# Optimization experiments

Hardware: AMD Instinct MI355X
Metric: run time of the kernel (lower is better)

Reference implementation:

```python
import jax, jax.numpy as jnp
import numpy as np

B, NQ, NK, D = 4, 512, 1024, 64
SCALE = 1.0


def _xavier(key, fan_in, fan_out):
    lim = np.sqrt(6.0 / (fan_in + fan_out))
    return jax.random.uniform(key, (fan_in, fan_out), jnp.float32, -lim, lim)


def setup_inputs() -> dict:
    key = jax.random.key(0)
    ks = jax.random.split(key, 7)
    return {
        "x1": jax.random.normal(ks[0], (B, NK, D), jnp.float32),   # context x -> keys
        "x2": jax.random.normal(ks[1], (B, NQ, D), jnp.float32),   # target x  -> queries
        "r":  jax.random.normal(ks[2], (B, NK, D), jnp.float32),   # values
        # key-path MLP (linear_layers_list): Linear(64,64) -> relu -> Linear(64,64)
        "Wk1": _xavier(ks[3], D, D), "bk1": jnp.zeros((D,), jnp.float32),
        "Wk2": _xavier(ks[4], D, D), "bk2": jnp.zeros((D,), jnp.float32),
        # query-path MLP (linear_layers_list2)
        "Wq1": _xavier(ks[5], D, D), "bq1": jnp.zeros((D,), jnp.float32),
        "Wq2": _xavier(ks[6], D, D), "bq2": jnp.zeros((D,), jnp.float32),
    }


def _mlp(x, W1, b1, W2, b2):
    # relu on all layers except the last (matches the torch loop)
    h = jax.nn.relu(jnp.einsum('bsd,de->bse', x, W1) + b1)
    return jnp.einsum('bsd,de->bse', h, W2) + b2


def reference(x1, x2, r, Wk1, bk1, Wk2, bk2, Wq1, bq1, Wq2, bq2):
    k = _mlp(x1, Wk1, bk1, Wk2, bk2)          # [B, NK, D]
    q = _mlp(x2, Wq1, bq1, Wq2, bq2)          # [B, NQ, D]
    # laplace attention: -sum_d |(k - q)/scale|, broadcast [B, NQ, NK, D]
    unnorm = -jnp.sum(jnp.abs((k[:, None, :, :] - q[:, :, None, :]) / SCALE), axis=-1)  # [B, NQ, NK]
    weights = jax.nn.softmax(unnorm, axis=2)  # normalise=True -> softmax over keys
    return jnp.einsum('bik,bkj->bij', weights, r)  # [B, NQ, D]
```

## Files before the change

kernel.cpp:

```cpp
#include <hip/hip_runtime.h>
#include <math.h>

#define BB 4
#define NQ 512
#define NK 1024
#define DH 64
#define TQ 8
#define TK 128
#define NCHUNK (NK / TK)
#define KPAD 65

__global__ __launch_bounds__(64) void mlp_kernel(
    const float* __restrict__ x1, const float* __restrict__ x2,
    const float* __restrict__ Wk1, const float* __restrict__ bk1,
    const float* __restrict__ Wk2, const float* __restrict__ bk2,
    const float* __restrict__ Wq1, const float* __restrict__ bq1,
    const float* __restrict__ Wq2, const float* __restrict__ bq2,
    float* __restrict__ kout, float* __restrict__ qout)
{
    const int row  = blockIdx.x;
    const int lane = threadIdx.x;
    const float *x, *W1, *b1, *W2, *b2;
    float* out;
    if (row < BB * NK) {
        x = x1 + row * DH;
        W1 = Wk1; b1 = bk1; W2 = Wk2; b2 = bk2;
        out = kout + row * DH;
    } else {
        const int rq = row - BB * NK;
        x = x2 + rq * DH;
        W1 = Wq1; b1 = bq1; W2 = Wq2; b2 = bq2;
        out = qout + rq * DH;
    }
    __shared__ float xs[DH];
    __shared__ float hs[DH];
    xs[lane] = x[lane];
    __syncthreads();
    float acc = b1[lane];
    #pragma unroll
    for (int d = 0; d < DH; ++d) acc = fmaf(xs[d], W1[d * DH + lane], acc);
    hs[lane] = fmaxf(acc, 0.0f);
    __syncthreads();
    float acc2 = b2[lane];
    #pragma unroll
    for (int d = 0; d < DH; ++d) acc2 = fmaf(hs[d], W2[d * DH + lane], acc2);
    out[lane] = acc2;
}

__global__ __launch_bounds__(512) void attn_kernel(
    const float* __restrict__ kmat, const float* __restrict__ qmat,
    const float* __restrict__ rmat, float* __restrict__ outp)
{
    __shared__ float k_s[TK * KPAD];
    __shared__ float p_s[TQ * TK];
    __shared__ float alpha_s[TQ];
    __shared__ float linv_s[TQ];

    const int t    = threadIdx.x;
    const int lane = t & 63;
    const int wav  = __builtin_amdgcn_readfirstlane(t >> 6);

    const int b  = blockIdx.x / (NQ / TQ);
    const int qt = blockIdx.x % (NQ / TQ);
    const int i0 = qt * TQ;

    const float* qrow = qmat + (b * NQ + i0 + wav) * DH;
    float qreg[DH];
    #pragma unroll
    for (int d = 0; d < DH; ++d) qreg[d] = qrow[d];

    const float* kbase = kmat + (size_t)b * NK * DH;
    const float* rbase = rmat + (size_t)b * NK * DH;

    float M_run = -INFINITY;
    float l_run = 0.0f;
    float O[TQ];
    #pragma unroll
    for (int i = 0; i < TQ; ++i) O[i] = 0.0f;

    for (int c = 0; c < NCHUNK; ++c) {
        const float4* ksrc = (const float4*)(kbase + c * TK * DH);
        #pragma unroll
        for (int rep = 0; rep < (TK * DH) / (512 * 4); ++rep) {
            int idx4 = rep * 512 + t;
            float4 v = ksrc[idx4];
            int e  = idx4 * 4;
            int jj = e >> 6;
            int dd = e & 63;
            float* dst = &k_s[jj * KPAD + dd];
            dst[0] = v.x; dst[1] = v.y; dst[2] = v.z; dst[3] = v.w;
        }
        __syncthreads();

        float s0 = 0.0f, s1 = 0.0f;
        #pragma unroll
        for (int d = 0; d < DH; ++d) {
            float q = qreg[d];
            s0 += fabsf(k_s[lane * KPAD + d] - q);
            s1 += fabsf(k_s[(lane + 64) * KPAD + d] - q);
        }
        float sm0 = -s0, sm1 = -s1;

        float cmax = fmaxf(sm0, sm1);
        #pragma unroll
        for (int off = 32; off > 0; off >>= 1)
            cmax = fmaxf(cmax, __shfl_xor(cmax, off, 64));
        float M_new = fmaxf(M_run, cmax);
        float p0 = __expf(sm0 - M_new);
        float p1 = __expf(sm1 - M_new);
        float csum = p0 + p1;
        #pragma unroll
        for (int off = 32; off > 0; off >>= 1)
            csum += __shfl_xor(csum, off, 64);
        float alpha = __expf(M_run - M_new);
        l_run = l_run * alpha + csum;
        M_run = M_new;
        p_s[wav * TK + lane]      = p0;
        p_s[wav * TK + lane + 64] = p1;
        if (lane == 0) alpha_s[wav] = alpha;
        __syncthreads();

        #pragma unroll
        for (int i = 0; i < TQ; ++i) O[i] *= alpha_s[i];
        const float* rc = rbase + c * TK * DH;
        #pragma unroll
        for (int jj = 0; jj < TK / 8; ++jj) {
            int j = wav * (TK / 8) + jj;
            float rv = rc[j * DH + lane];
            #pragma unroll
            for (int i = 0; i < TQ; ++i)
                O[i] = fmaf(p_s[i * TK + j], rv, O[i]);
        }
        __syncthreads();
    }

    if (lane == 0) linv_s[wav] = 1.0f / l_run;
    float* part = k_s;
    #pragma unroll
    for (int i = 0; i < TQ; ++i)
        part[(wav * TQ + i) * 64 + lane] = O[i];
    __syncthreads();

    float sum = 0.0f;
    #pragma unroll
    for (int g = 0; g < 8; ++g)
        sum += part[(g * TQ + wav) * 64 + lane];
    sum *= linv_s[wav];
    outp[((size_t)b * NQ + i0 + wav) * DH + lane] = sum;
}

extern "C" void kernel_launch(void* const* d_in, const int* in_sizes, int n_in,
                              void* d_out, int out_size, void* d_ws, size_t ws_size,
                              hipStream_t stream) {
    const float* x1  = (const float*)d_in[0];
    const float* x2  = (const float*)d_in[1];
    const float* r   = (const float*)d_in[2];
    const float* Wk1 = (const float*)d_in[3];
    const float* bk1 = (const float*)d_in[4];
    const float* Wk2 = (const float*)d_in[5];
    const float* bk2 = (const float*)d_in[6];
    const float* Wq1 = (const float*)d_in[7];
    const float* bq1 = (const float*)d_in[8];
    const float* Wq2 = (const float*)d_in[9];
    const float* bq2 = (const float*)d_in[10];
    float* out  = (float*)d_out;

    float* kbuf = (float*)d_ws;
    float* qbuf = kbuf + (size_t)BB * NK * DH;

    mlp_kernel<<<BB * (NK + NQ), 64, 0, stream>>>(
        x1, x2, Wk1, bk1, Wk2, bk2, Wq1, bq1, Wq2, bq2, kbuf, qbuf);

    attn_kernel<<<BB * (NQ / TQ), 512, 0, stream>>>(kbuf, qbuf, r, out);
}
```

Measured before the change: 111.1 us.

## Transpose K/Q layout and compute all scores per wave without online softmax

The MLP kernel now writes K and Q transposed (d-major), so the attention kernel can read K directly from global memory as coalesced float2 and reuse each K value across all 8 queries. The chunked online softmax with LDS staging of K is replaced by a single pass: each wave computes distances for 128 keys across 8 queries, a block-wide min reduction, and full exp into a 32KB p_s buffer, followed by a P·R pass. This removes per-chunk barriers and alpha rescaling and cuts the distance work from one query per wave to eight. In exchange the MLP stores become strided (uncoalesced), and the larger LDS footprint may lower occupancy.

```diff
diff --git a/kernel.cpp b/kernel.cpp
--- a/kernel.cpp
+++ b/kernel.cpp
@@ -6,9 +6,8 @@
 #define NK 1024
 #define DH 64
 #define TQ 8
-#define TK 128
-#define NCHUNK (NK / TK)
-#define KPAD 65
+#define NWAVE 8
+#define KPW (NK / NWAVE)
 
 __global__ __launch_bounds__(64) void mlp_kernel(
     const float* __restrict__ x1, const float* __restrict__ x2,
@@ -16,22 +15,26 @@
     const float* __restrict__ Wk2, const float* __restrict__ bk2,
     const float* __restrict__ Wq1, const float* __restrict__ bq1,
     const float* __restrict__ Wq2, const float* __restrict__ bq2,
-    float* __restrict__ kout, float* __restrict__ qout)
+    float* __restrict__ kT, float* __restrict__ qT)
 {
     const int row  = blockIdx.x;
     const int lane = threadIdx.x;
     const float *x, *W1, *b1, *W2, *b2;
     float* out;
     if (row < BB * NK) {
+        const int b = row / NK, j = row % NK;
         x = x1 + row * DH;
         W1 = Wk1; b1 = bk1; W2 = Wk2; b2 = bk2;
-        out = kout + row * DH;
+        out = kT + (size_t)b * DH * NK + j;
     } else {
         const int rq = row - BB * NK;
+        const int b = rq / NQ, i = rq % NQ;
         x = x2 + rq * DH;
         W1 = Wq1; b1 = bq1; W2 = Wq2; b2 = bq2;
-        out = qout + rq * DH;
+        out = qT + (size_t)b * DH * NQ + i;
     }
+    const int ostride = (row < BB * NK) ? NK : NQ;
+
     __shared__ float xs[DH];
     __shared__ float hs[DH];
     xs[lane] = x[lane];
@@ -44,98 +47,103 @@
     float acc2 = b2[lane];
     #pragma unroll
     for (int d = 0; d < DH; ++d) acc2 = fmaf(hs[d], W2[d * DH + lane], acc2);
-    out[lane] = acc2;
+    out[lane * ostride] = acc2;
 }
 
 __global__ __launch_bounds__(512) void attn_kernel(
-    const float* __restrict__ kmat, const float* __restrict__ qmat,
+    const float* __restrict__ kT, const float* __restrict__ qT,
     const float* __restrict__ rmat, float* __restrict__ outp)
 {
-    __shared__ float k_s[TK * KPAD];
-    __shared__ float p_s[TQ * TK];
-    __shared__ float alpha_s[TQ];
-    __shared__ float linv_s[TQ];
+    __shared__ float p_s[TQ * NK];
+    __shared__ float wmin_s[NWAVE * TQ];
+    __shared__ float wsum_s[NWAVE * TQ];
 
     const int t    = threadIdx.x;
     const int lane = t & 63;
     const int wav  = __builtin_amdgcn_readfirstlane(t >> 6);
 
     const int b  = blockIdx.x / (NQ / TQ);
-    const int qt = blockIdx.x % (NQ / TQ);
-    const int i0 = qt * TQ;
+    const int i0 = (blockIdx.x % (NQ / TQ)) * TQ;
 
-    const float* qrow = qmat + (b * NQ + i0 + wav) * DH;
-    float qreg[DH];
+    const float* kTb = kT + (size_t)b * DH * NK;
+    const float* qTb = qT + (size_t)b * DH * NQ;
+
+    const int j0 = wav * KPW + 2 * lane;
+
+    float s0[TQ], s1[TQ];
     #pragma unroll
-    for (int d = 0; d < DH; ++d) qreg[d] = qrow[d];
+    for (int i = 0; i < TQ; ++i) { s0[i] = 0.0f; s1[i] = 0.0f; }
 
-    const float* kbase = kmat + (size_t)b * NK * DH;
-    const float* rbase = rmat + (size_t)b * NK * DH;
+    #pragma unroll 8
+    for (int d = 0; d < DH; ++d) {
+        const float2 kv = *(const float2*)&kTb[d * NK + j0];
+        const float* qrow = qTb + d * NQ + i0;
+        #pragma unroll
+        for (int i = 0; i < TQ; ++i) {
+            const float q = qrow[i];
+            s0[i] += fabsf(kv.x - q);
+            s1[i] += fabsf(kv.y - q);
+        }
+    }
 
-    float M_run = -INFINITY;
-    float l_run = 0.0f;
+    #pragma unroll
+    for (int i = 0; i < TQ; ++i) {
+        float m = fminf(s0[i], s1[i]);
+        #pragma unroll
+        for (int off = 32; off > 0; off >>= 1)
+            m = fminf(m, __shfl_xor(m, off, 64));
+        if (lane == 0) wmin_s[wav * TQ + i] = m;
+    }
+    __syncthreads();
+
+    float M[TQ];
+    #pragma unroll
+    for (int i = 0; i < TQ; ++i) {
+        float m = wmin_s[i];
+        #pragma unroll
+        for (int g = 1; g < NWAVE; ++g) m = fminf(m, wmin_s[g * TQ + i]);
+        M[i] = m;
+    }
+
+    #pragma unroll
+    for (int i = 0; i < TQ; ++i) {
+        const float p0 = __expf(M[i] - s0[i]);
+        const float p1 = __expf(M[i] - s1[i]);
+        *(float2*)&p_s[i * NK + j0] = make_float2(p0, p1);
+        float cs = p0 + p1;
+        #pragma unroll
+        for (int off = 32; off > 0; off >>= 1)
+            cs += __shfl_xor(cs, off, 64);
+        if (lane == 0) wsum_s[wav * TQ + i] = cs;
+    }
+    __syncthreads();
+
+    float myl = 0.0f;
+    #pragma unroll
+    for (int g = 0; g < NWAVE; ++g) myl += wsum_s[g * TQ + wav];
+
     float O[TQ];
     #pragma unroll
     for (int i = 0; i < TQ; ++i) O[i] = 0.0f;
 
-    for (int c = 0; c < NCHUNK; ++c) {
-        const float4* ksrc = (const float4*)(kbase + c * TK * DH);
+    const float* rb = rmat + ((size_t)b * NK + wav * KPW) * DH;
+    for (int jj = 0; jj < KPW; jj += 4) {
+        const float rv0 = rb[(jj + 0) * DH + lane];
+        const float rv1 = rb[(jj + 1) * DH + lane];
+        const float rv2 = rb[(jj + 2) * DH + lane];
+        const float rv3 = rb[(jj + 3) * DH + lane];
         #pragma unroll
-        for (int rep = 0; rep < (TK * DH) / (512 * 4); ++rep) {
-            int idx4 = rep * 512 + t;
-            float4 v = ksrc[idx4];
-            int e  = idx4 * 4;
-            int jj = e >> 6;
-            int dd = e & 63;
-            float* dst = &k_s[jj * KPAD + dd];
-            dst[0] = v.x; dst[1] = v.y; dst[2] = v.z; dst[3] = v.w;
+        for (int i = 0; i < TQ; ++i) {
+            const float4 p4 = *(const float4*)&p_s[i * NK + wav * KPW + jj];
+            O[i] = fmaf(p4.x, rv0, O[i]);
+            O[i] = fmaf(p4.y, rv1, O[i]);
+            O[i] = fmaf(p4.z, rv2, O[i]);
+            O[i] = fmaf(p4.w, rv3, O[i]);
         }
-        __syncthreads();
+    }
+    __syncthreads();
 
-        float s0 = 0.0f, s1 = 0.0f;
-        #pragma unroll
-        for (int d = 0; d < DH; ++d) {
-            float q = qreg[d];
-            s0 += fabsf(k_s[lane * KPAD + d] - q);
-            s1 += fabsf(k_s[(lane + 64) * KPAD + d] - q);
-        }
-        float sm0 = -s0, sm1 = -s1;
-
-        float cmax = fmaxf(sm0, sm1);
-        #pragma unroll
-        for (int off = 32; off > 0; off >>= 1)
-            cmax = fmaxf(cmax, __shfl_xor(cmax, off, 64));
-        float M_new = fmaxf(M_run, cmax);
-        float p0 = __expf(sm0 - M_new);
-        float p1 = __expf(sm1 - M_new);
-        float csum = p0 + p1;
-        #pragma unroll
-        for (int off = 32; off > 0; off >>= 1)
-            csum += __shfl_xor(csum, off, 64);
-        float alpha = __expf(M_run - M_new);
-        l_run = l_run * alpha + csum;
-        M_run = M_new;
-        p_s[wav * TK + lane]      = p0;
-        p_s[wav * TK + lane + 64] = p1;
-        if (lane == 0) alpha_s[wav] = alpha;
-        __syncthreads();
-
-        #pragma unroll
-        for (int i = 0; i < TQ; ++i) O[i] *= alpha_s[i];
-        const float* rc = rbase + c * TK * DH;
-        #pragma unroll
-        for (int jj = 0; jj < TK / 8; ++jj) {
-            int j = wav * (TK / 8) + jj;
-            float rv = rc[j * DH + lane];
-            #pragma unroll
-            for (int i = 0; i < TQ; ++i)
-                O[i] = fmaf(p_s[i * TK + j], rv, O[i]);
-        }
-        __syncthreads();
-    }
-
-    if (lane == 0) linv_s[wav] = 1.0f / l_run;
-    float* part = k_s;
+    float* part = p_s;
     #pragma unroll
     for (int i = 0; i < TQ; ++i)
         part[(wav * TQ + i) * 64 + lane] = O[i];
@@ -143,10 +151,9 @@
 
     float sum = 0.0f;
     #pragma unroll
-    for (int g = 0; g < 8; ++g)
+    for (int g = 0; g < NWAVE; ++g)
         sum += part[(g * TQ + wav) * 64 + lane];
-    sum *= linv_s[wav];
-    outp[((size_t)b * NQ + i0 + wav) * DH + lane] = sum;
+    outp[((size_t)b * NQ + i0 + wav) * DH + lane] = sum / myl;
 }
 
 extern "C" void kernel_launch(void* const* d_in, const int* in_sizes, int n_in,
@@ -165,11 +172,11 @@
     const float* bq2 = (const float*)d_in[10];
     float* out  = (float*)d_out;
 
-    float* kbuf = (float*)d_ws;
-    float* qbuf = kbuf + (size_t)BB * NK * DH;
+    float* kT = (float*)d_ws;
+    float* qT = kT + (size_t)BB * DH * NK;
 
     mlp_kernel<<<BB * (NK + NQ), 64, 0, stream>>>(
-        x1, x2, Wk1, bk1, Wk2, bk2, Wq1, bq1, Wq2, bq2, kbuf, qbuf);
+        x1, x2, Wk1, bk1, Wk2, bk2, Wq1, bq1, Wq2, bq2, kT, qT);
 
-    attn_kernel<<<BB * (NQ / TQ), 512, 0, stream>>>(kbuf, qbuf, r, out);
+    attn_kernel<<<BB * (NQ / TQ), 512, 0, stream>>>(kT, qT, r, out);
 }
```

Result: faster. 108.3 us (-2.5%).
